# Optimization experiments

Hardware: AMD Instinct MI355X
Metric: run time of the kernel (lower is better)

Reference implementation:

```python
import jax, jax.numpy as jnp
import numpy as np

B, N, D = 256, 512, 64  # batch, positions, channels; units = spatial_units = D


def setup_inputs() -> dict:
    key = jax.random.key(0)
    ks = jax.random.split(key, 9)
    g = 1.0 / np.sqrt(D)  # glorot-ish scale for square matrices
    return {
        "x": jax.random.normal(ks[0], (B, N, D), dtype=jnp.float32),
        "Wq_t": jax.random.normal(ks[1], (D, D), dtype=jnp.float32) * g,
        "Wk_t": jax.random.normal(ks[2], (D, D), dtype=jnp.float32) * g,
        "Wv_t": jax.random.normal(ks[3], (D, D), dtype=jnp.float32) * g,
        "Wq_s": jax.random.normal(ks[4], (D, D), dtype=jnp.float32) * g,
        "Wk_s": jax.random.normal(ks[5], (D, D), dtype=jnp.float32) * g,
        "Wv_s": jax.random.normal(ks[6], (D, D), dtype=jnp.float32) * g,
        "Wd_t": jax.random.normal(ks[7], (D, D), dtype=jnp.float32) * g,
        "bd_t": jnp.zeros((D,), dtype=jnp.float32),
        "Wd_s": jax.random.normal(ks[8], (D, D), dtype=jnp.float32) * g,
        "bd_s": jnp.zeros((D,), dtype=jnp.float32),
    }


def _branch(x, Wq, Wk, Wv, Wd, bd):
    # x: [B, N, D]; one self-attention branch followed by a Dense layer.
    q = jnp.einsum("bnd,de->bne", x, Wq)
    k = jnp.einsum("bnd,de->bne", x, Wk)
    v = jnp.einsum("bnd,de->bne", x, Wv)
    scale = 1.0 / jnp.sqrt(jnp.asarray(Wk.shape[-1], dtype=x.dtype))
    scores = jnp.einsum("bne,bme->bnm", q, k) * scale  # [B, N, N]
    w = jax.nn.softmax(scores, axis=-1)
    attn = jnp.einsum("bnm,bmd->bnd", w, v)
    return jnp.einsum("bnd,de->bne", attn, Wd) + bd


def reference(x, Wq_t, Wk_t, Wv_t, Wq_s, Wk_s, Wv_s, Wd_t, bd_t, Wd_s, bd_s):
    temporal = _branch(x, Wq_t, Wk_t, Wv_t, Wd_t, bd_t)
    spatial = _branch(x, Wq_s, Wk_s, Wv_s, Wd_s, bd_s)
    gate = jax.nn.sigmoid(temporal + spatial)
    return x * gate
```

## Files before the change

### kernel.cpp

```cpp
#include <hip/hip_runtime.h>

typedef __attribute__((ext_vector_type(8))) short short8;
typedef __attribute__((ext_vector_type(4))) short short4v;
typedef __attribute__((ext_vector_type(4))) float float4v;

#define MFMA16(a, b, c) __builtin_amdgcn_mfma_f32_16x16x32_bf16((a), (b), (c), 0, 0, 0)

constexpr int kN = 512;
constexpr int kD = 64;
constexpr int kThreads = 1024;

constexpr int LDS_TOTAL_BYTES = 79872 * 2;

static __device__ __forceinline__ unsigned short f2bf(float f) {
  unsigned int u = __float_as_uint(f);
  u = (u + 0x7fffu + ((u >> 16) & 1u)) >> 16;
  return (unsigned short)u;
}

__global__ __launch_bounds__(kThreads, 4) void ts_attn_fused(
    const float* __restrict__ x, const float* __restrict__ Wq_t,
    const float* __restrict__ Wk_t, const float* __restrict__ Wv_t,
    const float* __restrict__ Wq_s, const float* __restrict__ Wk_s,
    const float* __restrict__ Wv_s, const float* __restrict__ Wd_t,
    const float* __restrict__ bd_t, const float* __restrict__ Wd_s,
    const float* __restrict__ bd_s, float* __restrict__ out) {
  extern __shared__ __align__(16) unsigned short smem_us[];
  unsigned short* Ksw = smem_us;
  unsigned short* Vsw = smem_us + 32768;
  unsigned short* Wdsw = smem_us + 65536;
  unsigned short* rep = smem_us + 69632;

  const int tid = threadIdx.x;
  const int wv = tid >> 6;
  const int lane = tid & 63;
  const int ln = lane & 15;
  const int quad = lane >> 4;
  const int b = blockIdx.x;

  const float* xb = x + (size_t)b * (kN * kD);
  float* outb = out + (size_t)b * (kN * kD);

  const int sd = tid >> 4;
  const int se0 = (tid & 15) * 4;
  const int sbase = (sd >> 3) * 512 + (sd & 7);

  float bdsum[4];
#pragma unroll
  for (int nt = 0; nt < 4; ++nt) bdsum[nt] = bd_t[nt * 16 + ln] + bd_s[nt * 16 + ln];

#pragma unroll 1
  for (int br = 0; br < 2; ++br) {
    const float* Wq = br ? Wq_s : Wq_t;
    const float* Wk = br ? Wk_s : Wk_t;
    const float* Wv = br ? Wv_s : Wv_t;
    const float* Wd = br ? Wd_s : Wd_t;

    {
      const float* srcs[3] = {Wq, Wk, Wv};
      unsigned short* dsts[3] = {rep, rep + 4096, Wdsw};
#pragma unroll
      for (int g = 0; g < 3; ++g) {
        const float4v u = *reinterpret_cast<const float4v*>(srcs[g] + sd * 64 + se0);
        unsigned short* dst = dsts[g];
#pragma unroll
        for (int i = 0; i < 4; ++i) dst[sbase + (se0 + i) * 8] = f2bf(u[i]);
      }
    }
    __syncthreads();

    short4v qd[2][4];
#pragma unroll 1
    for (int mi = 0; mi < 2; ++mi) {
      const int mt = wv + mi * 16;
      const int mrow = mt * 16 + ln;
      short8 xa0, xa1;
      {
        const float4v* p0 = reinterpret_cast<const float4v*>(xb + mrow * 64 + quad * 8);
        const float4v u0 = p0[0], v0 = p0[1];
        const float4v* p1 = reinterpret_cast<const float4v*>(xb + mrow * 64 + 32 + quad * 8);
        const float4v u1 = p1[0], v1 = p1[1];
#pragma unroll
        for (int i = 0; i < 4; ++i) {
          xa0[i] = (short)f2bf(u0[i]);
          xa0[4 + i] = (short)f2bf(v0[i]);
          xa1[i] = (short)f2bf(u1[i]);
          xa1[4 + i] = (short)f2bf(v1[i]);
        }
      }
#pragma unroll
      for (int g = 0; g < 3; ++g) {
        const unsigned short* Wl = (g == 0) ? rep : (g == 1) ? (rep + 4096) : Wdsw;
#pragma unroll
        for (int nt = 0; nt < 4; ++nt) {
          const short8 b0 = *reinterpret_cast<const short8*>(Wl + quad * 512 + (nt * 16 + ln) * 8);
          const short8 b1 =
              *reinterpret_cast<const short8*>(Wl + (4 + quad) * 512 + (nt * 16 + ln) * 8);
          float4v acc = {0.f, 0.f, 0.f, 0.f};
          acc = MFMA16(xa0, b0, acc);
          acc = MFMA16(xa1, b1, acc);
          if (g == 0) {
            short4v pk;
#pragma unroll
            for (int r = 0; r < 4; ++r) pk[r] = (short)f2bf(acc[r]);
            qd[mi][nt] = pk;
          } else if (g == 1) {
            const int ehi = nt * 2 + (ln >> 3);
            const int elo = ln & 7;
#pragma unroll
            for (int r = 0; r < 4; ++r)
              Ksw[ehi * 4096 + (mt * 16 + quad * 4 + r) * 8 + elo] = f2bf(acc[r]);
          } else {
            short4v pk;
#pragma unroll
            for (int r = 0; r < 4; ++r) pk[r] = (short)f2bf(acc[r]);
            const int vbase = (mt * 2 + (quad >> 1)) * 512 + (nt * 16 + ln) * 8 + (quad & 1) * 4;
            *reinterpret_cast<short4v*>(Vsw + vbase) = pk;
          }
        }
      }
    }
    __syncthreads();

    {
      const float4v u = *reinterpret_cast<const float4v*>(Wd + sd * 64 + se0);
#pragma unroll
      for (int i = 0; i < 4; ++i) Wdsw[sbase + (se0 + i) * 8] = f2bf(u[i]);
    }
    __syncthreads();

    unsigned short* buf = rep + wv * 640;
#pragma unroll 1
    for (int qi = 0; qi < 2; ++qi) {
      const int qt = wv + qi * 16;

      short8 q0, q1;
#pragma unroll
      for (int nt = 0; nt < 2; ++nt)
#pragma unroll
        for (int r = 0; r < 4; ++r)
          buf[(quad * 4 + r) * 40 + nt * 16 + ln] = (unsigned short)qd[qi][nt][r];
      asm volatile("s_waitcnt lgkmcnt(0)" ::: "memory");
      q0 = *reinterpret_cast<const short8*>(buf + ln * 40 + quad * 8);
#pragma unroll
      for (int nt = 2; nt < 4; ++nt)
#pragma unroll
        for (int r = 0; r < 4; ++r)
          buf[(quad * 4 + r) * 40 + (nt - 2) * 16 + ln] = (unsigned short)qd[qi][nt][r];
      asm volatile("s_waitcnt lgkmcnt(0)" ::: "memory");
      q1 = *reinterpret_cast<const short8*>(buf + ln * 40 + quad * 8);

      float sum[4] = {0.f, 0.f, 0.f, 0.f};
      float4v o[4];
#pragma unroll
      for (int i = 0; i < 4; ++i) o[i] = (float4v){0.f, 0.f, 0.f, 0.f};

#pragma unroll 1
      for (int sc = 0; sc < 4; ++sc) {
        float4v s[8];
#pragma unroll
        for (int t = 0; t < 8; ++t) {
          const int nt = sc * 8 + t;
          const short8 k0 =
              *reinterpret_cast<const short8*>(Ksw + quad * 4096 + (nt * 16 + ln) * 8);
          const short8 k1 =
              *reinterpret_cast<const short8*>(Ksw + (4 + quad) * 4096 + (nt * 16 + ln) * 8);
          float4v acc = {0.f, 0.f, 0.f, 0.f};
          acc = MFMA16(q0, k0, acc);
          acc = MFMA16(q1, k1, acc);
          s[t] = acc;
        }
#pragma unroll
        for (int kc2 = 0; kc2 < 4; ++kc2) {
          const int kcg = sc * 4 + kc2;
#pragma unroll
          for (int t2 = 0; t2 < 2; ++t2) {
            const float4v sv = s[kc2 * 2 + t2];
#pragma unroll
            for (int r = 0; r < 4; ++r) {
              const float p = __expf(sv[r] * 0.125f);
              sum[r] += p;
              buf[(quad * 4 + r) * 40 + t2 * 16 + ln] = f2bf(p);
            }
          }
          asm volatile("s_waitcnt lgkmcnt(0)" ::: "memory");
          const short8 pa = *reinterpret_cast<const short8*>(buf + ln * 40 + quad * 8);
#pragma unroll
          for (int nto = 0; nto < 4; ++nto) {
            const short8 vf =
                *reinterpret_cast<const short8*>(Vsw + (kcg * 4 + quad) * 512 + (nto * 16 + ln) * 8);
            o[nto] = MFMA16(pa, vf, o[nto]);
          }
        }
      }

#pragma unroll
      for (int dd = 1; dd < 16; dd <<= 1)
#pragma unroll
        for (int r = 0; r < 4; ++r) sum[r] += __shfl_xor(sum[r], dd, 64);
      float inv[4];
#pragma unroll
      for (int r = 0; r < 4; ++r) inv[r] = 1.0f / sum[r];

#pragma unroll
      for (int nto = 0; nto < 2; ++nto)
#pragma unroll
        for (int r = 0; r < 4; ++r)
          buf[(quad * 4 + r) * 40 + nto * 16 + ln] = f2bf(o[nto][r] * inv[r]);
      asm volatile("s_waitcnt lgkmcnt(0)" ::: "memory");
      const short8 a0 = *reinterpret_cast<const short8*>(buf + ln * 40 + quad * 8);
#pragma unroll
      for (int nto = 2; nto < 4; ++nto)
#pragma unroll
        for (int r = 0; r < 4; ++r)
          buf[(quad * 4 + r) * 40 + (nto - 2) * 16 + ln] = f2bf(o[nto][r] * inv[r]);
      asm volatile("s_waitcnt lgkmcnt(0)" ::: "memory");
      const short8 a1 = *reinterpret_cast<const short8*>(buf + ln * 40 + quad * 8);

#pragma unroll
      for (int nt = 0; nt < 4; ++nt) {
        const short8 w0 = *reinterpret_cast<const short8*>(Wdsw + quad * 512 + (nt * 16 + ln) * 8);
        const short8 w1 =
            *reinterpret_cast<const short8*>(Wdsw + (4 + quad) * 512 + (nt * 16 + ln) * 8);
        float4v d4 = {0.f, 0.f, 0.f, 0.f};
        d4 = MFMA16(a0, w0, d4);
        d4 = MFMA16(a1, w1, d4);
        const int m0 = qt * 16 + quad * 4;
        const int col = nt * 16 + ln;
        if (br == 0) {
#pragma unroll
          for (int r = 0; r < 4; ++r) outb[(m0 + r) * 64 + col] = d4[r];
        } else {
#pragma unroll
          for (int r = 0; r < 4; ++r) {
            const float z = outb[(m0 + r) * 64 + col] + d4[r] + bdsum[nt];
            const float gate = 1.0f / (1.0f + __expf(-z));
            outb[(m0 + r) * 64 + col] = xb[(m0 + r) * 64 + col] * gate;
          }
        }
      }
    }
    __syncthreads();
  }
}

extern "C" void kernel_launch(void* const* d_in, const int* in_sizes, int n_in,
                              void* d_out, int out_size, void* d_ws, size_t ws_size,
                              hipStream_t stream) {
  const float* x = (const float*)d_in[0];
  const float* Wq_t = (const float*)d_in[1];
  const float* Wk_t = (const float*)d_in[2];
  const float* Wv_t = (const float*)d_in[3];
  const float* Wq_s = (const float*)d_in[4];
  const float* Wk_s = (const float*)d_in[5];
  const float* Wv_s = (const float*)d_in[6];
  const float* Wd_t = (const float*)d_in[7];
  const float* bd_t = (const float*)d_in[8];
  const float* Wd_s = (const float*)d_in[9];
  const float* bd_s = (const float*)d_in[10];
  float* out = (float*)d_out;

  hipFuncSetAttribute(reinterpret_cast<const void*>(ts_attn_fused),
                      hipFuncAttributeMaxDynamicSharedMemorySize, LDS_TOTAL_BYTES);
  ts_attn_fused<<<dim3(256), dim3(kThreads), LDS_TOTAL_BYTES, stream>>>(
      x, Wq_t, Wk_t, Wv_t, Wq_s, Wk_s, Wv_s, Wd_t, bd_t, Wd_s, bd_s, out);
}
```

Baseline: 205.6 us.

## Process both query tiles per wave together to share K/V/W fragment loads

Each wave now handles its two 16-row query tiles at the same time instead of one after the other, in the projection, score, PV and output-dense stages. Every K, V and weight fragment read from LDS is reused for two MFMAs, which halves LDS read traffic and gives the scheduler more independent MFMA work. The change also swaps scalar bf16 conversion for the packed two-wide intrinsic and replaces the explicit lgkmcnt waits with compiler-only memory fences. The cost is more live registers for the doubled accumulators and scores, which may hurt occupancy. Dropping the explicit waits relies on the compiler inserting correct waits for the round trip through the shared buffer.

```diff
diff --git a/kernel.cpp b/kernel.cpp
--- a/kernel.cpp
+++ b/kernel.cpp
@@ -1,10 +1,12 @@
 #include <hip/hip_runtime.h>
+#include <hip/hip_bf16.h>
 
 typedef __attribute__((ext_vector_type(8))) short short8;
 typedef __attribute__((ext_vector_type(4))) short short4v;
 typedef __attribute__((ext_vector_type(4))) float float4v;
 
 #define MFMA16(a, b, c) __builtin_amdgcn_mfma_f32_16x16x32_bf16((a), (b), (c), 0, 0, 0)
+#define LDS_FENCE() asm volatile("" ::: "memory")
 
 constexpr int kN = 512;
 constexpr int kD = 64;
@@ -17,6 +19,20 @@
   u = (u + 0x7fffu + ((u >> 16) & 1u)) >> 16;
   return (unsigned short)u;
 }
+
+static __device__ __forceinline__ unsigned int f2bf2(float a, float b) {
+  union {
+    __hip_bfloat162 h;
+    unsigned int u;
+  } cvt;
+  cvt.h = __float22bfloat162_rn(float2{a, b});
+  return cvt.u;
+}
+
+union S8U4 {
+  short8 s8;
+  unsigned int u4[4];
+};
 
 __global__ __launch_bounds__(kThreads, 4) void ts_attn_fused(
     const float* __restrict__ x, const float* __restrict__ Wq_t,
@@ -69,36 +85,42 @@
     }
     __syncthreads();
 
+    short8 xa[2][2];
+#pragma unroll
+    for (int mi = 0; mi < 2; ++mi) {
+      const int mrow = (wv + mi * 16) * 16 + ln;
+      const float4v u0 = *reinterpret_cast<const float4v*>(xb + mrow * 64 + quad * 8);
+      const float4v v0 = *reinterpret_cast<const float4v*>(xb + mrow * 64 + quad * 8 + 4);
+      const float4v u1 = *reinterpret_cast<const float4v*>(xb + mrow * 64 + 32 + quad * 8);
+      const float4v v1 = *reinterpret_cast<const float4v*>(xb + mrow * 64 + 32 + quad * 8 + 4);
+      S8U4 t0, t1;
+      t0.u4[0] = f2bf2(u0[0], u0[1]);
+      t0.u4[1] = f2bf2(u0[2], u0[3]);
+      t0.u4[2] = f2bf2(v0[0], v0[1]);
+      t0.u4[3] = f2bf2(v0[2], v0[3]);
+      t1.u4[0] = f2bf2(u1[0], u1[1]);
+      t1.u4[1] = f2bf2(u1[2], u1[3]);
+      t1.u4[2] = f2bf2(v1[0], v1[1]);
+      t1.u4[3] = f2bf2(v1[2], v1[3]);
+      xa[mi][0] = t0.s8;
+      xa[mi][1] = t1.s8;
+    }
+
     short4v qd[2][4];
-#pragma unroll 1
-    for (int mi = 0; mi < 2; ++mi) {
-      const int mt = wv + mi * 16;
-      const int mrow = mt * 16 + ln;
-      short8 xa0, xa1;
-      {
-        const float4v* p0 = reinterpret_cast<const float4v*>(xb + mrow * 64 + quad * 8);
-        const float4v u0 = p0[0], v0 = p0[1];
-        const float4v* p1 = reinterpret_cast<const float4v*>(xb + mrow * 64 + 32 + quad * 8);
-        const float4v u1 = p1[0], v1 = p1[1];
-#pragma unroll
-        for (int i = 0; i < 4; ++i) {
-          xa0[i] = (short)f2bf(u0[i]);
-          xa0[4 + i] = (short)f2bf(v0[i]);
-          xa1[i] = (short)f2bf(u1[i]);
-          xa1[4 + i] = (short)f2bf(v1[i]);
-        }
-      }
-#pragma unroll
-      for (int g = 0; g < 3; ++g) {
-        const unsigned short* Wl = (g == 0) ? rep : (g == 1) ? (rep + 4096) : Wdsw;
-#pragma unroll
-        for (int nt = 0; nt < 4; ++nt) {
-          const short8 b0 = *reinterpret_cast<const short8*>(Wl + quad * 512 + (nt * 16 + ln) * 8);
-          const short8 b1 =
-              *reinterpret_cast<const short8*>(Wl + (4 + quad) * 512 + (nt * 16 + ln) * 8);
+#pragma unroll
+    for (int g = 0; g < 3; ++g) {
+      const unsigned short* Wl = (g == 0) ? rep : (g == 1) ? (rep + 4096) : Wdsw;
+#pragma unroll
+      for (int nt = 0; nt < 4; ++nt) {
+        const short8 b0 = *reinterpret_cast<const short8*>(Wl + quad * 512 + (nt * 16 + ln) * 8);
+        const short8 b1 =
+            *reinterpret_cast<const short8*>(Wl + (4 + quad) * 512 + (nt * 16 + ln) * 8);
+#pragma unroll
+        for (int mi = 0; mi < 2; ++mi) {
+          const int mt = wv + mi * 16;
           float4v acc = {0.f, 0.f, 0.f, 0.f};
-          acc = MFMA16(xa0, b0, acc);
-          acc = MFMA16(xa1, b1, acc);
+          acc = MFMA16(xa[mi][0], b0, acc);
+          acc = MFMA16(xa[mi][1], b1, acc);
           if (g == 0) {
             short4v pk;
 #pragma unroll
@@ -130,103 +152,120 @@
     __syncthreads();
 
     unsigned short* buf = rep + wv * 640;
+
+    short8 q[2][2];
+#pragma unroll
+    for (int u = 0; u < 2; ++u) {
+#pragma unroll
+      for (int p = 0; p < 2; ++p) {
+#pragma unroll
+        for (int h = 0; h < 2; ++h)
+#pragma unroll
+          for (int r = 0; r < 4; ++r)
+            buf[(quad * 4 + r) * 40 + h * 16 + ln] = (unsigned short)qd[u][p * 2 + h][r];
+        LDS_FENCE();
+        q[u][p] = *reinterpret_cast<const short8*>(buf + ln * 40 + quad * 8);
+        LDS_FENCE();
+      }
+    }
+
+    float sum[2][4];
+    float4v o[2][4];
+#pragma unroll
+    for (int u = 0; u < 2; ++u)
+#pragma unroll
+      for (int i = 0; i < 4; ++i) {
+        sum[u][i] = 0.f;
+        o[u][i] = (float4v){0.f, 0.f, 0.f, 0.f};
+      }
+
 #pragma unroll 1
-    for (int qi = 0; qi < 2; ++qi) {
-      const int qt = wv + qi * 16;
-
-      short8 q0, q1;
-#pragma unroll
-      for (int nt = 0; nt < 2; ++nt)
-#pragma unroll
-        for (int r = 0; r < 4; ++r)
-          buf[(quad * 4 + r) * 40 + nt * 16 + ln] = (unsigned short)qd[qi][nt][r];
-      asm volatile("s_waitcnt lgkmcnt(0)" ::: "memory");
-      q0 = *reinterpret_cast<const short8*>(buf + ln * 40 + quad * 8);
-#pragma unroll
-      for (int nt = 2; nt < 4; ++nt)
-#pragma unroll
-        for (int r = 0; r < 4; ++r)
-          buf[(quad * 4 + r) * 40 + (nt - 2) * 16 + ln] = (unsigned short)qd[qi][nt][r];
-      asm volatile("s_waitcnt lgkmcnt(0)" ::: "memory");
-      q1 = *reinterpret_cast<const short8*>(buf + ln * 40 + quad * 8);
-
-      float sum[4] = {0.f, 0.f, 0.f, 0.f};
-      float4v o[4];
-#pragma unroll
-      for (int i = 0; i < 4; ++i) o[i] = (float4v){0.f, 0.f, 0.f, 0.f};
-
-#pragma unroll 1
-      for (int sc = 0; sc < 4; ++sc) {
-        float4v s[8];
-#pragma unroll
-        for (int t = 0; t < 8; ++t) {
-          const int nt = sc * 8 + t;
-          const short8 k0 =
-              *reinterpret_cast<const short8*>(Ksw + quad * 4096 + (nt * 16 + ln) * 8);
-          const short8 k1 =
-              *reinterpret_cast<const short8*>(Ksw + (4 + quad) * 4096 + (nt * 16 + ln) * 8);
+    for (int sc = 0; sc < 8; ++sc) {
+      float4v s[2][4];
+#pragma unroll
+      for (int t = 0; t < 4; ++t) {
+        const int nt = sc * 4 + t;
+        const short8 k0 = *reinterpret_cast<const short8*>(Ksw + quad * 4096 + (nt * 16 + ln) * 8);
+        const short8 k1 =
+            *reinterpret_cast<const short8*>(Ksw + (4 + quad) * 4096 + (nt * 16 + ln) * 8);
+#pragma unroll
+        for (int u = 0; u < 2; ++u) {
           float4v acc = {0.f, 0.f, 0.f, 0.f};
-          acc = MFMA16(q0, k0, acc);
-          acc = MFMA16(q1, k1, acc);
-          s[t] = acc;
-        }
-#pragma unroll
-        for (int kc2 = 0; kc2 < 4; ++kc2) {
-          const int kcg = sc * 4 + kc2;
+          acc = MFMA16(q[u][0], k0, acc);
+          acc = MFMA16(q[u][1], k1, acc);
+          s[u][t] = acc;
+        }
+      }
+#pragma unroll
+      for (int kc2 = 0; kc2 < 2; ++kc2) {
+        const int kcg = sc * 2 + kc2;
+        short8 pa[2];
+#pragma unroll
+        for (int u = 0; u < 2; ++u) {
 #pragma unroll
           for (int t2 = 0; t2 < 2; ++t2) {
-            const float4v sv = s[kc2 * 2 + t2];
+            const float4v sv = s[u][kc2 * 2 + t2];
 #pragma unroll
             for (int r = 0; r < 4; ++r) {
               const float p = __expf(sv[r] * 0.125f);
-              sum[r] += p;
+              sum[u][r] += p;
               buf[(quad * 4 + r) * 40 + t2 * 16 + ln] = f2bf(p);
             }
           }
-          asm volatile("s_waitcnt lgkmcnt(0)" ::: "memory");
-          const short8 pa = *reinterpret_cast<const short8*>(buf + ln * 40 + quad * 8);
-#pragma unroll
-          for (int nto = 0; nto < 4; ++nto) {
-            const short8 vf =
-                *reinterpret_cast<const short8*>(Vsw + (kcg * 4 + quad) * 512 + (nto * 16 + ln) * 8);
-            o[nto] = MFMA16(pa, vf, o[nto]);
-          }
-        }
-      }
-
-#pragma unroll
-      for (int dd = 1; dd < 16; dd <<= 1)
-#pragma unroll
-        for (int r = 0; r < 4; ++r) sum[r] += __shfl_xor(sum[r], dd, 64);
-      float inv[4];
-#pragma unroll
-      for (int r = 0; r < 4; ++r) inv[r] = 1.0f / sum[r];
-
-#pragma unroll
-      for (int nto = 0; nto < 2; ++nto)
-#pragma unroll
-        for (int r = 0; r < 4; ++r)
-          buf[(quad * 4 + r) * 40 + nto * 16 + ln] = f2bf(o[nto][r] * inv[r]);
-      asm volatile("s_waitcnt lgkmcnt(0)" ::: "memory");
-      const short8 a0 = *reinterpret_cast<const short8*>(buf + ln * 40 + quad * 8);
-#pragma unroll
-      for (int nto = 2; nto < 4; ++nto)
-#pragma unroll
-        for (int r = 0; r < 4; ++r)
-          buf[(quad * 4 + r) * 40 + (nto - 2) * 16 + ln] = f2bf(o[nto][r] * inv[r]);
-      asm volatile("s_waitcnt lgkmcnt(0)" ::: "memory");
-      const short8 a1 = *reinterpret_cast<const short8*>(buf + ln * 40 + quad * 8);
-
-#pragma unroll
-      for (int nt = 0; nt < 4; ++nt) {
-        const short8 w0 = *reinterpret_cast<const short8*>(Wdsw + quad * 512 + (nt * 16 + ln) * 8);
-        const short8 w1 =
-            *reinterpret_cast<const short8*>(Wdsw + (4 + quad) * 512 + (nt * 16 + ln) * 8);
+          LDS_FENCE();
+          pa[u] = *reinterpret_cast<const short8*>(buf + ln * 40 + quad * 8);
+          LDS_FENCE();
+        }
+#pragma unroll
+        for (int nto = 0; nto < 4; ++nto) {
+          const short8 vf =
+              *reinterpret_cast<const short8*>(Vsw + (kcg * 4 + quad) * 512 + (nto * 16 + ln) * 8);
+          o[0][nto] = MFMA16(pa[0], vf, o[0][nto]);
+          o[1][nto] = MFMA16(pa[1], vf, o[1][nto]);
+        }
+      }
+    }
+
+#pragma unroll
+    for (int dd = 1; dd < 16; dd <<= 1)
+#pragma unroll
+      for (int u = 0; u < 2; ++u)
+#pragma unroll
+        for (int r = 0; r < 4; ++r) sum[u][r] += __shfl_xor(sum[u][r], dd, 64);
+    float inv[2][4];
+#pragma unroll
+    for (int u = 0; u < 2; ++u)
+#pragma unroll
+      for (int r = 0; r < 4; ++r) inv[u][r] = 1.0f / sum[u][r];
+
+    short8 a[2][2];
+#pragma unroll
+    for (int u = 0; u < 2; ++u) {
+#pragma unroll
+      for (int p = 0; p < 2; ++p) {
+#pragma unroll
+        for (int h = 0; h < 2; ++h)
+#pragma unroll
+          for (int r = 0; r < 4; ++r)
+            buf[(quad * 4 + r) * 40 + h * 16 + ln] = f2bf(o[u][p * 2 + h][r] * inv[u][r]);
+        LDS_FENCE();
+        a[u][p] = *reinterpret_cast<const short8*>(buf + ln * 40 + quad * 8);
+        LDS_FENCE();
+      }
+    }
+
+#pragma unroll
+    for (int nt = 0; nt < 4; ++nt) {
+      const short8 w0 = *reinterpret_cast<const short8*>(Wdsw + quad * 512 + (nt * 16 + ln) * 8);
+      const short8 w1 =
+          *reinterpret_cast<const short8*>(Wdsw + (4 + quad) * 512 + (nt * 16 + ln) * 8);
+      const int col = nt * 16 + ln;
+#pragma unroll
+      for (int u = 0; u < 2; ++u) {
         float4v d4 = {0.f, 0.f, 0.f, 0.f};
-        d4 = MFMA16(a0, w0, d4);
-        d4 = MFMA16(a1, w1, d4);
-        const int m0 = qt * 16 + quad * 4;
-        const int col = nt * 16 + ln;
+        d4 = MFMA16(a[u][0], w0, d4);
+        d4 = MFMA16(a[u][1], w1, d4);
+        const int m0 = (wv + u * 16) * 16 + quad * 4;
         if (br == 0) {
 #pragma unroll
           for (int r = 0; r < 4; ++r) outb[(m0 + r) * 64 + col] = d4[r];
```

Measured after the change: 211.5 us. 2.9% more time.
